# Kernel tuning notes

Hardware: AMD Instinct MI355X
Metric: run time of the kernel (lower is better)

Reference implementation:

```python
import jax, jax.numpy as jnp
import numpy as np

E = 8          # num_experts
K = 2          # top_k
CF = 1.5       # capacity_factor
THR = 0.5      # imp_threshold
EPS = 1e-9


def setup_inputs() -> dict:
    key = jax.random.key(0)
    ks = jax.random.split(key, 14)
    B, S, H = 2, 2048, 2048

    def w(k, shape, fan_in):
        return jax.random.normal(k, shape, jnp.float32) * (1.0 / np.sqrt(fan_in))

    return {
        "hidden_states": jax.random.normal(ks[0], (B, S, H), jnp.float32),
        # importance predictor: Linear(H, H//2) -> ReLU -> Linear(H//2, 1) -> Sigmoid
        "Wi1": w(ks[1], (H, H // 2), H), "bi1": jnp.zeros((H // 2,), jnp.float32),
        "Wi2": w(ks[2], (H // 2, 1), H // 2), "bi2": jnp.zeros((1,), jnp.float32),
        # router_important: Linear(H, H) -> ReLU -> Linear(H, E)
        "Wr1": w(ks[3], (H, H), H), "br1": jnp.zeros((H,), jnp.float32),
        "Wr2": w(ks[4], (H, E), H), "br2": jnp.zeros((E,), jnp.float32),
        # router_unimportant: Linear(H, H) -> ReLU -> Linear(H, E)
        "Wu1": w(ks[5], (H, H), H), "bu1": jnp.zeros((H,), jnp.float32),
        "Wu2": w(ks[6], (H, E), H), "bu2": jnp.zeros((E,), jnp.float32),
    }


def _dispatch_combine(top_idx, top_p, capacity):
    # top_idx, top_p: [T, K].  Faithfully reproduces the torch loop, including
    # index_put (non-accumulating) semantics for expert_count updates: within a
    # top-k slot, every token routed to expert e reads the same stale count and
    # the count advances by at most 1 per expert per slot.
    T = top_idx.shape[0]
    disp = jnp.zeros((T, E, capacity), top_p.dtype)
    comb = jnp.zeros((T, E, capacity), top_p.dtype)
    count = jnp.zeros((E,), jnp.int32)
    tok = jnp.arange(T)
    for i in range(K):
        e = top_idx[:, i]            # [T]
        p = top_p[:, i]              # [T]
        pos = count[e]               # stale gather, [T]
        mask = pos < capacity
        pos_c = jnp.where(mask, pos, 0)
        # (tok, e) pairs are unique across slots (top-k indices are distinct),
        # so masked zero-writes never clobber earlier ones.
        disp = disp.at[tok, e, pos_c].set(mask.astype(disp.dtype))
        comb = comb.at[tok, e, pos_c].set(jnp.where(mask, p, jnp.zeros_like(p)))
        occ = jax.ops.segment_sum(mask.astype(jnp.int32), e, num_segments=E) > 0
        count = count + occ.astype(jnp.int32)
    return disp, comb


def _mlp2(x, W1, b1, W2, b2):
    return jax.nn.relu(x @ W1 + b1) @ W2 + b2


def reference(hidden_states, Wi1, bi1, Wi2, bi2, Wr1, br1, Wr2, br2, Wu1, bu1, Wu2, bu2):
    B, S, H = hidden_states.shape
    x = hidden_states

    importance = jax.nn.sigmoid(_mlp2(x, Wi1, bi1, Wi2, bi2))          # [B,S,1]
    imp_mask = (importance > THR).astype(x.dtype)                       # [B,S,1]

    logits_imp = _mlp2(x, Wr1, br1, Wr2, br2)                           # [B,S,E]
    logits_unimp = _mlp2(x, Wu1, bu1, Wu2, bu2)                         # [B,S,E]
    router_logits = imp_mask * logits_imp + (1.0 - imp_mask) * logits_unimp

    router_probs = jax.nn.softmax(router_logits, axis=-1)               # [B,S,E]
    top_p, top_idx = jax.lax.top_k(router_probs, K)                     # [B,S,K]
    top_p = top_p / top_p.sum(-1, keepdims=True)

    capacity = int(B * S * CF * K / E)
    T = B * S
    disp, comb = _dispatch_combine(top_idx.reshape(T, K), top_p.reshape(T, K), capacity)
    disp = disp.reshape(B, S, E, capacity)
    comb = comb.reshape(B, S, E, capacity)

    rppe = router_probs.mean(axis=(0, 1))                               # [E]
    entropy_loss = jnp.sum(rppe * jnp.log(rppe * E + EPS))

    imp_sum = (router_probs * imp_mask).sum(axis=(0, 1)) + EPS          # [E]
    ipe = imp_sum / imp_sum.sum()
    imp_entropy = -jnp.sum(ipe * jnp.log(ipe + EPS))
    aux_loss = entropy_loss - 0.1 * (imp_entropy / np.log(E))

    return (disp, comb, router_probs, aux_loss, importance)
```

## Files before the change

### kernel.cpp

```cpp
#include <hip/hip_runtime.h>
#include <math.h>

#define M_TOK 4096
#define HID   2048
#define NEXP  8
#define CAP   1536
#define DISP_ELEMS 50331648ull
#define NTOT  5120
#define ZTOT4 25165824ull

typedef __attribute__((ext_vector_type(8))) short bf16x8;
typedef __attribute__((ext_vector_type(4))) float f32x4;

__device__ __forceinline__ unsigned short f2bf(float f) {
  unsigned u = __float_as_uint(f);
  unsigned r = u + 0x7FFFu + ((u >> 16) & 1u);
  return (unsigned short)(r >> 16);
}
__device__ __forceinline__ float bf2f(unsigned short h) {
  return __uint_as_float(((unsigned)h) << 16);
}

__device__ __forceinline__ void gload16(const void* g, void* l) {
  __builtin_amdgcn_global_load_lds(
      (const __attribute__((address_space(1))) void*)g,
      (__attribute__((address_space(3))) void*)l, 16, 0, 0);
}
__device__ __forceinline__ bf16x8 ldsread(const unsigned short* p) {
  return *reinterpret_cast<const bf16x8*>(p);
}

__global__ __launch_bounds__(256)
void convert_x_k(const float* __restrict__ x, unsigned short* __restrict__ xh,
                 unsigned short* __restrict__ xl) {
  size_t i = ((size_t)blockIdx.x * 256 + threadIdx.x) * 4;
  float4 v = *reinterpret_cast<const float4*>(&x[i]);
  float f[4] = {v.x, v.y, v.z, v.w};
  unsigned short hh[4], ll[4];
#pragma unroll
  for (int j = 0; j < 4; ++j) {
    hh[j] = f2bf(f[j]);
    ll[j] = f2bf(f[j] - bf2f(hh[j]));
  }
  uint2 ph, pl;
  ph.x = hh[0] | ((unsigned)hh[1] << 16); ph.y = hh[2] | ((unsigned)hh[3] << 16);
  pl.x = ll[0] | ((unsigned)ll[1] << 16); pl.y = ll[2] | ((unsigned)ll[3] << 16);
  *reinterpret_cast<uint2*>(&xh[i]) = ph;
  *reinterpret_cast<uint2*>(&xl[i]) = pl;
}

__global__ __launch_bounds__(256)
void convert_wT_k(const float* __restrict__ Wi1, const float* __restrict__ Wr1,
                  const float* __restrict__ Wu1,
                  unsigned short* __restrict__ wTh,
                  unsigned short* __restrict__ wTl) {
  __shared__ float tile[32][33];
  const int bx = blockIdx.x;
  const float* W; int N, rowOff, nb;
  if (bx < 32)      { W = Wi1; N = 1024; rowOff = 0;    nb = bx; }
  else if (bx < 96) { W = Wr1; N = 2048; rowOff = 1024; nb = bx - 32; }
  else              { W = Wu1; N = 2048; rowOff = 3072; nb = bx - 96; }
  const int k0 = blockIdx.y * 32;
  const int n0 = nb * 32;
  const int tid = threadIdx.x;
  {
    int r = tid >> 3, c4 = (tid & 7) * 4;
    float4 v = *reinterpret_cast<const float4*>(&W[(size_t)(k0 + r) * N + n0 + c4]);
    tile[r][c4 + 0] = v.x; tile[r][c4 + 1] = v.y;
    tile[r][c4 + 2] = v.z; tile[r][c4 + 3] = v.w;
  }
  __syncthreads();
  int n = tid >> 3, kc = (tid & 7) * 4;
  unsigned short hh[4], ll[4];
#pragma unroll
  for (int j = 0; j < 4; ++j) {
    float f = tile[kc + j][n];
    hh[j] = f2bf(f);
    ll[j] = f2bf(f - bf2f(hh[j]));
  }
  size_t o = (size_t)(rowOff + n0 + n) * HID + k0 + kc;
  uint2 ph, pl;
  ph.x = hh[0] | ((unsigned)hh[1] << 16); ph.y = hh[2] | ((unsigned)hh[3] << 16);
  pl.x = ll[0] | ((unsigned)ll[1] << 16); pl.y = ll[2] | ((unsigned)ll[3] << 16);
  *reinterpret_cast<uint2*>(&wTh[o]) = ph;
  *reinterpret_cast<uint2*>(&wTl[o]) = pl;
}

__global__ __launch_bounds__(512, 2)
void gemm_split_k(const unsigned short* __restrict__ Ahg,
                  const unsigned short* __restrict__ Alg,
                  const unsigned short* __restrict__ Bhg,
                  const unsigned short* __restrict__ Blg,
                  const float* __restrict__ bi1, const float* __restrict__ br1,
                  const float* __restrict__ bu1, float* __restrict__ h_i,
                  float* __restrict__ h_r, float* __restrict__ h_u,
                  float* __restrict__ dzero) {
  __shared__ unsigned short lds[73728];
  const int bid  = blockIdx.x;
  const int tid  = threadIdx.x;
  const int lane = tid & 63;
  const int wave = tid >> 6;
  const int lr   = lane & 15;
  const int slot = lane >> 4;

  const int idx = bid >> 3;
  const int mt  = ((bid & 7) << 1) | (idx >> 4);
  const int nt  = idx & 15;
  const int row0  = mt * 256;
  const int bcol0 = nt * 320;

  const unsigned short* gsrc[9];
#pragma unroll
  for (int j = 0; j < 9; ++j) {
    int c = (wave * 9 + j) * 64 + lane;
    const unsigned short* base;
    int sidx, rowg;
    if (c < 2048) {
      sidx = c & 1023;
      base = (c < 1024) ? Ahg : Alg;
      rowg = row0 + (sidx >> 2);
    } else {
      sidx = (c < 3328) ? (c - 2048) : (c - 3328);
      base = (c < 3328) ? Bhg : Blg;
      rowg = bcol0 + (sidx >> 2);
    }
    int q  = sidx & 3;
    int qs = q ^ (((sidx >> 2) >> 1) & 3);
    gsrc[j] = base + (size_t)rowg * HID + qs * 8;
  }
  const int ldsbase = wave * 4608 + lane * 8;

  int aoff[8], boff[5];
#pragma unroll
  for (int m = 0; m < 8; ++m) {
    int ra = (wave >> 2) * 128 + m * 16 + lr;
    aoff[m] = ra * 32 + (slot ^ ((ra >> 1) & 3)) * 8;
  }
#pragma unroll
  for (int n = 0; n < 5; ++n) {
    int rb = (wave & 3) * 80 + n * 16 + lr;
    boff[n] = rb * 32 + (slot ^ ((rb >> 1) & 3)) * 8;
  }

  f32x4 acc[8][5];
#pragma unroll
  for (int m = 0; m < 8; ++m)
#pragma unroll
    for (int n = 0; n < 5; ++n) acc[m][n] = (f32x4){0.f, 0.f, 0.f, 0.f};

  auto stage = [&](int kt, unsigned short* buf) {
#pragma unroll
    for (int j = 0; j < 9; ++j)
      gload16(gsrc[j] + kt * 32, buf + ldsbase + j * 512);
  };
  auto computeTile = [&](const unsigned short* bb) {
    bf16x8 bvh[5], bvl[5];
#pragma unroll
    for (int n = 0; n < 5; ++n) {
      bvh[n] = ldsread(&bb[16384 + boff[n]]);
      bvl[n] = ldsread(&bb[26624 + boff[n]]);
    }
#pragma unroll
    for (int m = 0; m < 8; ++m) {
      bf16x8 ah = ldsread(&bb[aoff[m]]);
      bf16x8 al = ldsread(&bb[8192 + aoff[m]]);
      __builtin_amdgcn_s_setprio(1);
#pragma unroll
      for (int n = 0; n < 5; ++n) {
        acc[m][n] = __builtin_amdgcn_mfma_f32_16x16x32_bf16(ah, bvh[n], acc[m][n], 0, 0, 0);
        acc[m][n] = __builtin_amdgcn_mfma_f32_16x16x32_bf16(ah, bvl[n], acc[m][n], 0, 0, 0);
        acc[m][n] = __builtin_amdgcn_mfma_f32_16x16x32_bf16(al, bvh[n], acc[m][n], 0, 0, 0);
      }
      __builtin_amdgcn_s_setprio(0);
    }
  };

  unsigned short* b0 = &lds[0];
  unsigned short* b1 = &lds[36864];
  const bool dz = (dzero != nullptr);
  f32x4* d4 = (f32x4*)dzero;
  const f32x4 zv = (f32x4){0.f, 0.f, 0.f, 0.f};

  stage(0, b0);

#pragma unroll 1
  for (int t = 0; t < 64; ++t) {
    unsigned short* cur = (t & 1) ? b1 : b0;
    unsigned short* nxt = (t & 1) ? b0 : b1;
    if (t < 63) stage(t + 1, nxt);
    if (dz) {
      size_t zb = ((size_t)(bid * 64 + t) * 3) * 512 + tid;
      __builtin_nontemporal_store(zv, d4 + zb);
      __builtin_nontemporal_store(zv, d4 + zb + 512);
      __builtin_nontemporal_store(zv, d4 + zb + 1024);
    }
    if (t < 63) {
      if (dz) asm volatile("s_waitcnt vmcnt(12)" ::: "memory");
      else    asm volatile("s_waitcnt vmcnt(9)"  ::: "memory");
    } else {
      if (dz) asm volatile("s_waitcnt vmcnt(3)"  ::: "memory");
      else    asm volatile("s_waitcnt vmcnt(0)"  ::: "memory");
    }
    __builtin_amdgcn_s_barrier();
    __builtin_amdgcn_sched_barrier(0);
    computeTile(cur);
    __builtin_amdgcn_s_barrier();
  }

#pragma unroll
  for (int n = 0; n < 5; ++n) {
    int cbase = nt * 320 + (wave & 3) * 80 + n * 16;
    float* C; const float* bias; int ldc, coff;
    if (cbase < 1024)      { C = h_i; bias = bi1; ldc = 1024; coff = 0; }
    else if (cbase < 3072) { C = h_r; bias = br1; ldc = 2048; coff = 1024; }
    else                   { C = h_u; bias = bu1; ldc = 2048; coff = 3072; }
    int cl = cbase - coff + lr;
    float bn = bias[cl];
#pragma unroll
    for (int m = 0; m < 8; ++m) {
      int rbase = row0 + (wave >> 2) * 128 + m * 16 + slot * 4;
#pragma unroll
      for (int j = 0; j < 4; ++j)
        C[(size_t)(rbase + j) * ldc + cl] = fmaxf(acc[m][n][j] + bn, 0.f);
    }
  }
}

__global__ __launch_bounds__(256)
void router_k(const float* __restrict__ h_i, const float* __restrict__ h_r,
              const float* __restrict__ h_u,
              const float* __restrict__ Wi2, const float* __restrict__ bi2,
              const float* __restrict__ Wr2, const float* __restrict__ br2,
              const float* __restrict__ Wu2, const float* __restrict__ bu2,
              float* __restrict__ router_probs, float* __restrict__ importance,
              int* __restrict__ expert_used) {
  __shared__ float wr[18432];
  __shared__ float wu[18432];
  __shared__ float wi[1024];
  const int tid = threadIdx.x;

  for (int idx = tid; idx < 16384; idx += 256)
    wr[(idx >> 3) * 9 + (idx & 7)] = Wr2[idx];
  for (int idx = tid; idx < 16384; idx += 256)
    wu[(idx >> 3) * 9 + (idx & 7)] = Wu2[idx];
  for (int idx = tid; idx < 1024; idx += 256) wi[idx] = Wi2[idx];
  __syncthreads();

  const int w = tid >> 6, l = tid & 63;
  const float bi2v = bi2[0];

#pragma unroll 1
  for (int tt = 0; tt < 4; ++tt) {
    const int t = blockIdx.x * 16 + tt * 4 + w;
    float acc[17];
#pragma unroll
    for (int k = 0; k < 17; ++k) acc[k] = 0.f;

    const float* hi = &h_i[(size_t)t * 1024];
    const float* hr = &h_r[(size_t)t * 2048];
    const float* hu = &h_u[(size_t)t * 2048];
#pragma unroll 4
    for (int j = 0; j < 16; ++j) {
      int k = j * 64 + l;
      acc[0] = fmaf(hi[k], wi[k], acc[0]);
    }
#pragma unroll 4
    for (int j = 0; j < 32; ++j) {
      int k = j * 64 + l;
      float hrv = hr[k], huv = hu[k];
      const float* wrr = &wr[k * 9];
      const float* wuu = &wu[k * 9];
#pragma unroll
      for (int e = 0; e < 8; ++e) {
        acc[1 + e] = fmaf(hrv, wrr[e], acc[1 + e]);
        acc[9 + e] = fmaf(huv, wuu[e], acc[9 + e]);
      }
    }
#pragma unroll
    for (int k = 0; k < 17; ++k) {
      float v = acc[k];
      v += __shfl_xor(v, 1);  v += __shfl_xor(v, 2);  v += __shfl_xor(v, 4);
      v += __shfl_xor(v, 8);  v += __shfl_xor(v, 16); v += __shfl_xor(v, 32);
      acc[k] = v;
    }
    if (l == 0) {
      float imp = 1.f / (1.f + expf(-(acc[0] + bi2v)));
      importance[t] = imp;
      bool useImp = imp > 0.5f;
      float logits[8];
#pragma unroll
      for (int e = 0; e < 8; ++e)
        logits[e] = useImp ? (acc[1 + e] + br2[e]) : (acc[9 + e] + bu2[e]);
      float mx = logits[0];
#pragma unroll
      for (int e = 1; e < 8; ++e) mx = fmaxf(mx, logits[e]);
      float ex[8], sum = 0.f;
#pragma unroll
      for (int e = 0; e < 8; ++e) { ex[e] = expf(logits[e] - mx); sum += ex[e]; }
      float p[8];
#pragma unroll
      for (int e = 0; e < 8; ++e) p[e] = ex[e] / sum;
#pragma unroll
      for (int e = 0; e < 8; ++e) router_probs[(size_t)t * 8 + e] = p[e];
      int e1 = 0; float p1 = p[0];
#pragma unroll
      for (int e = 1; e < 8; ++e) if (p[e] > p1) { p1 = p[e]; e1 = e; }
      expert_used[e1] = 1;
    }
  }
}

__global__ __launch_bounds__(256)
void scatter_aux_k(const float* __restrict__ router_probs,
                   const int* __restrict__ expert_used,
                   const float* __restrict__ importance,
                   float* __restrict__ disp, float* __restrict__ comb,
                   float* __restrict__ partials) {
  const int tid = threadIdx.x;
  const int t = blockIdx.x * 256 + tid;
  float4 a = *reinterpret_cast<const float4*>(&router_probs[(size_t)t * 8]);
  float4 b = *reinterpret_cast<const float4*>(&router_probs[(size_t)t * 8 + 4]);
  float p[8] = {a.x, a.y, a.z, a.w, b.x, b.y, b.z, b.w};
  int e1 = 0; float p1 = p[0];
#pragma unroll
  for (int e = 1; e < 8; ++e) if (p[e] > p1) { p1 = p[e]; e1 = e; }
  int e2 = 0; float p2 = -1.f;
#pragma unroll
  for (int e = 0; e < 8; ++e) {
    if (e == e1) continue;
    if (p[e] > p2) { p2 = p[e]; e2 = e; }
  }
  float s = p1 + p2;
  size_t base = (size_t)t * NEXP * CAP;
  disp[base + (size_t)e1 * CAP + 0] = 1.f;
  comb[base + (size_t)e1 * CAP + 0] = p1 / s;
  int pos = expert_used[e2];
  disp[base + (size_t)e2 * CAP + pos] = 1.f;
  comb[base + (size_t)e2 * CAP + pos] = p2 / s;

  float mk = importance[t] > 0.5f ? 1.f : 0.f;
  float vals[16];
#pragma unroll
  for (int e = 0; e < 8; ++e) { vals[e] = p[e]; vals[8 + e] = p[e] * mk; }
#pragma unroll
  for (int k = 0; k < 16; ++k) {
    float v = vals[k];
    v += __shfl_xor(v, 1);  v += __shfl_xor(v, 2);  v += __shfl_xor(v, 4);
    v += __shfl_xor(v, 8);  v += __shfl_xor(v, 16); v += __shfl_xor(v, 32);
    vals[k] = v;
  }
  __shared__ float red[4][16];
  const int lane = tid & 63, wid = tid >> 6;
  if (lane == 0) {
#pragma unroll
    for (int k = 0; k < 16; ++k) red[wid][k] = vals[k];
  }
  __syncthreads();
  if (tid < 16)
    atomicAdd(&partials[tid],
              red[0][tid] + red[1][tid] + red[2][tid] + red[3][tid]);
}

__global__ __launch_bounds__(64)
void aux_final_k(float* __restrict__ partials, float* __restrict__ aux_out,
                 float* __restrict__ flag_tail) {
  const int tid = threadIdx.x;
  float s[16];
#pragma unroll
  for (int k = 0; k < 16; ++k) s[k] = partials[k];
  if (tid == 0) {
    float entropy_loss = 0.f;
#pragma unroll
    for (int e = 0; e < 8; ++e) {
      float rppe = s[e] / (float)M_TOK;
      entropy_loss += rppe * logf(rppe * 8.f + 1e-9f);
    }
    float tot = 0.f;
#pragma unroll
    for (int e = 0; e < 8; ++e) tot += s[8 + e] + 1e-9f;
    float imp_entropy = 0.f;
#pragma unroll
    for (int e = 0; e < 8; ++e) {
      float ipe = (s[8 + e] + 1e-9f) / tot;
      imp_entropy -= ipe * logf(ipe + 1e-9f);
    }
    aux_out[0] = entropy_loss - 0.1f * (imp_entropy / logf(8.f));
  }
  if (tid < 16) partials[tid] = 0.f;
  if (tid >= 16 && tid < 32) flag_tail[tid - 16] = 0.f;
}

extern "C" void kernel_launch(void* const* d_in, const int* in_sizes, int n_in,
                              void* d_out, int out_size, void* d_ws,
                              size_t ws_size, hipStream_t stream) {
  const float* x   = (const float*)d_in[0];
  const float* Wi1 = (const float*)d_in[1];
  const float* bi1 = (const float*)d_in[2];
  const float* Wi2 = (const float*)d_in[3];
  const float* bi2 = (const float*)d_in[4];
  const float* Wr1 = (const float*)d_in[5];
  const float* br1 = (const float*)d_in[6];
  const float* Wr2 = (const float*)d_in[7];
  const float* br2 = (const float*)d_in[8];
  const float* Wu1 = (const float*)d_in[9];
  const float* bu1 = (const float*)d_in[10];
  const float* Wu2 = (const float*)d_in[11];
  const float* bu2 = (const float*)d_in[12];

  float* out  = (float*)d_out;
  float* disp = out;
  float* comb = out + DISP_ELEMS;
  float* rp   = out + 2 * DISP_ELEMS;
  float* aux  = out + 2 * DISP_ELEMS + 32768;
  float* imp  = aux + 1;

  const size_t xh_b  = (size_t)M_TOK * HID * 2;
  const size_t wT_b  = (size_t)NTOT * HID * 2;
  const size_t hi_b  = (size_t)M_TOK * 1024 * 4;
  const size_t hr_b  = (size_t)M_TOK * 2048 * 4;
  const size_t need  = 2 * xh_b + 2 * wT_b + hi_b + 2 * hr_b + 256;
  const bool ws_ok = (ws_size >= need);
  char* scratch = ws_ok ? (char*)d_ws : (char*)comb;

  unsigned short* xh  = (unsigned short*)scratch;
  unsigned short* xl  = (unsigned short*)(scratch + xh_b);
  unsigned short* wTh = (unsigned short*)(scratch + 2 * xh_b);
  unsigned short* wTl = (unsigned short*)(scratch + 2 * xh_b + wT_b);
  float* h_i = (float*)(scratch + 2 * xh_b + 2 * wT_b);
  float* h_r = h_i + (size_t)M_TOK * 1024;
  float* h_u = h_r + (size_t)M_TOK * 2048;
  int*   flags    = (int*)(comb + DISP_ELEMS - 16);
  float* partials = comb + DISP_ELEMS - 48;

  if (!ws_ok) {
    (void)hipMemsetAsync(disp, 0, DISP_ELEMS * sizeof(float), stream);
    (void)hipMemsetAsync(flags, 0, 16 * sizeof(float), stream);
  }

  convert_x_k<<<(M_TOK * HID / 4) / 256, 256, 0, stream>>>(x, xh, xl);
  convert_wT_k<<<dim3(160, HID / 32), 256, 0, stream>>>(Wi1, Wr1, Wu1, wTh, wTl);

  gemm_split_k<<<256, 512, 0, stream>>>(xh, xl, wTh, wTl, bi1, br1, bu1,
                                        h_i, h_r, h_u,
                                        ws_ok ? disp : (float*)nullptr);

  router_k<<<256, 256, 0, stream>>>(h_i, h_r, h_u, Wi2, bi2, Wr2, br2,
                                    Wu2, bu2, rp, imp, flags);

  if (!ws_ok)
    (void)hipMemsetAsync(comb, 0, (DISP_ELEMS - 16) * sizeof(float), stream);

  scatter_aux_k<<<M_TOK / 256, 256, 0, stream>>>(rp, flags, imp, disp, comb,
                                                 partials);

  aux_final_k<<<1, 64, 0, stream>>>(partials, aux, (float*)flags);
}
```

Measured before the change: 292.6 us.

## Shrink GEMM tile to 128 rows, single-buffer LDS, raise occupancy, fuse convert kernels

The split-bf16 GEMM tile is halved from 256 to 128 rows, launching 512 blocks instead of 256. Shared memory drops to a single buffer so four blocks can fit per CU, relying on occupancy instead of double buffering to hide load latency. Each K-step now waits for all loads, computes in three passes (hi*hi, hi*lo, lo*hi), then issues the next stage, with the disp zeroing stores redistributed across iterations. The two conversion kernels are merged into one launch. The cost is a full load stall every iteration and more redundant B-tile loads across the extra blocks.

Result: slower. 301.4 us (+3.0%).

```diff
diff --git a/kernel.cpp b/kernel.cpp
--- a/kernel.cpp
+++ b/kernel.cpp
@@ -31,38 +31,41 @@
 }
 
 __global__ __launch_bounds__(256)
-void convert_x_k(const float* __restrict__ x, unsigned short* __restrict__ xh,
-                 unsigned short* __restrict__ xl) {
-  size_t i = ((size_t)blockIdx.x * 256 + threadIdx.x) * 4;
-  float4 v = *reinterpret_cast<const float4*>(&x[i]);
-  float f[4] = {v.x, v.y, v.z, v.w};
-  unsigned short hh[4], ll[4];
-#pragma unroll
-  for (int j = 0; j < 4; ++j) {
-    hh[j] = f2bf(f[j]);
-    ll[j] = f2bf(f[j] - bf2f(hh[j]));
-  }
-  uint2 ph, pl;
-  ph.x = hh[0] | ((unsigned)hh[1] << 16); ph.y = hh[2] | ((unsigned)hh[3] << 16);
-  pl.x = ll[0] | ((unsigned)ll[1] << 16); pl.y = ll[2] | ((unsigned)ll[3] << 16);
-  *reinterpret_cast<uint2*>(&xh[i]) = ph;
-  *reinterpret_cast<uint2*>(&xl[i]) = pl;
-}
-
-__global__ __launch_bounds__(256)
-void convert_wT_k(const float* __restrict__ Wi1, const float* __restrict__ Wr1,
-                  const float* __restrict__ Wu1,
-                  unsigned short* __restrict__ wTh,
-                  unsigned short* __restrict__ wTl) {
+void convert_k(const float* __restrict__ x,
+               const float* __restrict__ Wi1, const float* __restrict__ Wr1,
+               const float* __restrict__ Wu1,
+               unsigned short* __restrict__ xh, unsigned short* __restrict__ xl,
+               unsigned short* __restrict__ wTh,
+               unsigned short* __restrict__ wTl) {
+  const int bid = blockIdx.x;
+  const int tid = threadIdx.x;
+  if (bid < 8192) {
+    size_t i = ((size_t)bid * 256 + tid) * 4;
+    float4 v = *reinterpret_cast<const float4*>(&x[i]);
+    float f[4] = {v.x, v.y, v.z, v.w};
+    unsigned short hh[4], ll[4];
+#pragma unroll
+    for (int j = 0; j < 4; ++j) {
+      hh[j] = f2bf(f[j]);
+      ll[j] = f2bf(f[j] - bf2f(hh[j]));
+    }
+    uint2 ph, pl;
+    ph.x = hh[0] | ((unsigned)hh[1] << 16); ph.y = hh[2] | ((unsigned)hh[3] << 16);
+    pl.x = ll[0] | ((unsigned)ll[1] << 16); pl.y = ll[2] | ((unsigned)ll[3] << 16);
+    *reinterpret_cast<uint2*>(&xh[i]) = ph;
+    *reinterpret_cast<uint2*>(&xl[i]) = pl;
+    return;
+  }
   __shared__ float tile[32][33];
-  const int bx = blockIdx.x;
+  const int wb = bid - 8192;
+  const int by = wb / 160;
+  const int bx = wb - by * 160;
   const float* W; int N, rowOff, nb;
   if (bx < 32)      { W = Wi1; N = 1024; rowOff = 0;    nb = bx; }
   else if (bx < 96) { W = Wr1; N = 2048; rowOff = 1024; nb = bx - 32; }
   else              { W = Wu1; N = 2048; rowOff = 3072; nb = bx - 96; }
-  const int k0 = blockIdx.y * 32;
+  const int k0 = by * 32;
   const int n0 = nb * 32;
-  const int tid = threadIdx.x;
   {
     int r = tid >> 3, c4 = (tid & 7) * 4;
     float4 v = *reinterpret_cast<const float4*>(&W[(size_t)(k0 + r) * N + n0 + c4]);
@@ -86,7 +89,7 @@
   *reinterpret_cast<uint2*>(&wTl[o]) = pl;
 }
 
-__global__ __launch_bounds__(512, 2)
+__global__ __launch_bounds__(512, 4)
 void gemm_split_k(const unsigned short* __restrict__ Ahg,
                   const unsigned short* __restrict__ Alg,
                   const unsigned short* __restrict__ Bhg,
@@ -95,7 +98,7 @@
                   const float* __restrict__ bu1, float* __restrict__ h_i,
                   float* __restrict__ h_r, float* __restrict__ h_u,
                   float* __restrict__ dzero) {
-  __shared__ unsigned short lds[73728];
+  __shared__ unsigned short lds[28672];
   const int bid  = blockIdx.x;
   const int tid  = threadIdx.x;
   const int lane = tid & 63;
@@ -104,36 +107,37 @@
   const int slot = lane >> 4;
 
   const int idx = bid >> 3;
-  const int mt  = ((bid & 7) << 1) | (idx >> 4);
-  const int nt  = idx & 15;
-  const int row0  = mt * 256;
+  const int nt  = (bid & 7) * 2 + (idx >> 5);
+  const int mt  = idx & 31;
+  const int row0  = mt * 128;
   const int bcol0 = nt * 320;
 
-  const unsigned short* gsrc[9];
-#pragma unroll
-  for (int j = 0; j < 9; ++j) {
-    int c = (wave * 9 + j) * 64 + lane;
+  const unsigned short* gsrc[7];
+#pragma unroll
+  for (int j = 0; j < 7; ++j) {
+    int cb = wave * 7 + j;
+    int c  = cb * 64 + lane;
     const unsigned short* base;
     int sidx, rowg;
-    if (c < 2048) {
-      sidx = c & 1023;
-      base = (c < 1024) ? Ahg : Alg;
-      rowg = row0 + (sidx >> 2);
+    if (cb < 8) {
+      sidx = c; base = Ahg; rowg = row0 + (sidx >> 2);
+    } else if (cb < 16) {
+      sidx = c - 512; base = Alg; rowg = row0 + (sidx >> 2);
+    } else if (cb < 36) {
+      sidx = c - 1024; base = Bhg; rowg = bcol0 + (sidx >> 2);
     } else {
-      sidx = (c < 3328) ? (c - 2048) : (c - 3328);
-      base = (c < 3328) ? Bhg : Blg;
-      rowg = bcol0 + (sidx >> 2);
+      sidx = c - 2304; base = Blg; rowg = bcol0 + (sidx >> 2);
     }
     int q  = sidx & 3;
     int qs = q ^ (((sidx >> 2) >> 1) & 3);
     gsrc[j] = base + (size_t)rowg * HID + qs * 8;
   }
-  const int ldsbase = wave * 4608 + lane * 8;
-
-  int aoff[8], boff[5];
-#pragma unroll
-  for (int m = 0; m < 8; ++m) {
-    int ra = (wave >> 2) * 128 + m * 16 + lr;
+  const int ldsbase = (wave * 7) * 512 + lane * 8;
+
+  int aoff[4], boff[5];
+#pragma unroll
+  for (int m = 0; m < 4; ++m) {
+    int ra = (wave >> 2) * 64 + m * 16 + lr;
     aoff[m] = ra * 32 + (slot ^ ((ra >> 1) & 3)) * 8;
   }
 #pragma unroll
@@ -142,69 +146,76 @@
     boff[n] = rb * 32 + (slot ^ ((rb >> 1) & 3)) * 8;
   }
 
-  f32x4 acc[8][5];
-#pragma unroll
-  for (int m = 0; m < 8; ++m)
+  f32x4 acc[4][5];
+#pragma unroll
+  for (int m = 0; m < 4; ++m)
 #pragma unroll
     for (int n = 0; n < 5; ++n) acc[m][n] = (f32x4){0.f, 0.f, 0.f, 0.f};
 
-  auto stage = [&](int kt, unsigned short* buf) {
-#pragma unroll
-    for (int j = 0; j < 9; ++j)
-      gload16(gsrc[j] + kt * 32, buf + ldsbase + j * 512);
+  auto stage = [&](int kt) {
+#pragma unroll
+    for (int j = 0; j < 7; ++j)
+      gload16(gsrc[j] + kt * 32, &lds[ldsbase + j * 512]);
   };
-  auto computeTile = [&](const unsigned short* bb) {
-    bf16x8 bvh[5], bvl[5];
-#pragma unroll
-    for (int n = 0; n < 5; ++n) {
-      bvh[n] = ldsread(&bb[16384 + boff[n]]);
-      bvl[n] = ldsread(&bb[26624 + boff[n]]);
-    }
-#pragma unroll
-    for (int m = 0; m < 8; ++m) {
-      bf16x8 ah = ldsread(&bb[aoff[m]]);
-      bf16x8 al = ldsread(&bb[8192 + aoff[m]]);
-      __builtin_amdgcn_s_setprio(1);
-#pragma unroll
-      for (int n = 0; n < 5; ++n) {
-        acc[m][n] = __builtin_amdgcn_mfma_f32_16x16x32_bf16(ah, bvh[n], acc[m][n], 0, 0, 0);
-        acc[m][n] = __builtin_amdgcn_mfma_f32_16x16x32_bf16(ah, bvl[n], acc[m][n], 0, 0, 0);
-        acc[m][n] = __builtin_amdgcn_mfma_f32_16x16x32_bf16(al, bvh[n], acc[m][n], 0, 0, 0);
-      }
-      __builtin_amdgcn_s_setprio(0);
-    }
-  };
-
-  unsigned short* b0 = &lds[0];
-  unsigned short* b1 = &lds[36864];
+
   const bool dz = (dzero != nullptr);
   f32x4* d4 = (f32x4*)dzero;
   const f32x4 zv = (f32x4){0.f, 0.f, 0.f, 0.f};
-
-  stage(0, b0);
+  const size_t zbase = (size_t)bid * 49152 + tid;
+
+  stage(0);
 
 #pragma unroll 1
   for (int t = 0; t < 64; ++t) {
-    unsigned short* cur = (t & 1) ? b1 : b0;
-    unsigned short* nxt = (t & 1) ? b0 : b1;
-    if (t < 63) stage(t + 1, nxt);
-    if (dz) {
-      size_t zb = ((size_t)(bid * 64 + t) * 3) * 512 + tid;
-      __builtin_nontemporal_store(zv, d4 + zb);
-      __builtin_nontemporal_store(zv, d4 + zb + 512);
-      __builtin_nontemporal_store(zv, d4 + zb + 1024);
-    }
-    if (t < 63) {
-      if (dz) asm volatile("s_waitcnt vmcnt(12)" ::: "memory");
-      else    asm volatile("s_waitcnt vmcnt(9)"  ::: "memory");
-    } else {
-      if (dz) asm volatile("s_waitcnt vmcnt(3)"  ::: "memory");
-      else    asm volatile("s_waitcnt vmcnt(0)"  ::: "memory");
-    }
+    asm volatile("s_waitcnt vmcnt(0)" ::: "memory");
     __builtin_amdgcn_s_barrier();
     __builtin_amdgcn_sched_barrier(0);
-    computeTile(cur);
+
+    bf16x8 bv[5];
+#pragma unroll
+    for (int n = 0; n < 5; ++n) bv[n] = ldsread(&lds[8192 + boff[n]]);
+#pragma unroll
+    for (int m = 0; m < 4; ++m) {
+      bf16x8 a = ldsread(&lds[aoff[m]]);
+      __builtin_amdgcn_s_setprio(1);
+#pragma unroll
+      for (int n = 0; n < 5; ++n)
+        acc[m][n] = __builtin_amdgcn_mfma_f32_16x16x32_bf16(a, bv[n], acc[m][n], 0, 0, 0);
+      __builtin_amdgcn_s_setprio(0);
+    }
+#pragma unroll
+    for (int n = 0; n < 5; ++n) bv[n] = ldsread(&lds[18432 + boff[n]]);
+#pragma unroll
+    for (int m = 0; m < 4; ++m) {
+      bf16x8 a = ldsread(&lds[aoff[m]]);
+      __builtin_amdgcn_s_setprio(1);
+#pragma unroll
+      for (int n = 0; n < 5; ++n)
+        acc[m][n] = __builtin_amdgcn_mfma_f32_16x16x32_bf16(a, bv[n], acc[m][n], 0, 0, 0);
+      __builtin_amdgcn_s_setprio(0);
+    }
+#pragma unroll
+    for (int n = 0; n < 5; ++n) bv[n] = ldsread(&lds[8192 + boff[n]]);
+#pragma unroll
+    for (int m = 0; m < 4; ++m) {
+      bf16x8 a = ldsread(&lds[4096 + aoff[m]]);
+      __builtin_amdgcn_s_setprio(1);
+#pragma unroll
+      for (int n = 0; n < 5; ++n)
+        acc[m][n] = __builtin_amdgcn_mfma_f32_16x16x32_bf16(a, bv[n], acc[m][n], 0, 0, 0);
+      __builtin_amdgcn_s_setprio(0);
+    }
+
+    if (dz) {
+      int start = (3 * t) >> 1;
+      int cnt   = ((3 * (t + 1)) >> 1) - start;
+      __builtin_nontemporal_store(zv, d4 + zbase + (size_t)start * 512);
+      if (cnt == 2)
+        __builtin_nontemporal_store(zv, d4 + zbase + (size_t)(start + 1) * 512);
+    }
+
     __builtin_amdgcn_s_barrier();
+    if (t < 63) stage(t + 1);
   }
 
 #pragma unroll
@@ -217,8 +228,8 @@
     int cl = cbase - coff + lr;
     float bn = bias[cl];
 #pragma unroll
-    for (int m = 0; m < 8; ++m) {
-      int rbase = row0 + (wave >> 2) * 128 + m * 16 + slot * 4;
+    for (int m = 0; m < 4; ++m) {
+      int rbase = row0 + (wave >> 2) * 64 + m * 16 + slot * 4;
 #pragma unroll
       for (int j = 0; j < 4; ++j)
         C[(size_t)(rbase + j) * ldc + cl] = fmaxf(acc[m][n][j] + bn, 0.f);
@@ -437,10 +448,9 @@
     (void)hipMemsetAsync(flags, 0, 16 * sizeof(float), stream);
   }
 
-  convert_x_k<<<(M_TOK * HID / 4) / 256, 256, 0, stream>>>(x, xh, xl);
-  convert_wT_k<<<dim3(160, HID / 32), 256, 0, stream>>>(Wi1, Wr1, Wu1, wTh, wTl);
-
-  gemm_split_k<<<256, 512, 0, stream>>>(xh, xl, wTh, wTl, bi1, br1, bu1,
+  convert_k<<<18432, 256, 0, stream>>>(x, Wi1, Wr1, Wu1, xh, xl, wTh, wTl);
+
+  gemm_split_k<<<512, 512, 0, stream>>>(xh, xl, wTh, wTl, bi1, br1, bu1,
                                         h_i, h_r, h_u,
                                         ws_ok ? disp : (float*)nullptr);
 
```
